# Kernel optimization log

Measured on AMD Instinct MI355X. Metric: run time of the kernel, lower is better.

The kernel has to match this reference:

```python
import jax, jax.numpy as jnp
import numpy as np
import math

B, N, C = 4, 4096, 1024
H, K_LM = 16, 256
HEAD_DIM = C // H


def setup_inputs() -> dict:
    key = jax.random.key(0)
    k1, k2, k3, k4, k5 = jax.random.split(key, 5)
    x = jax.random.normal(k1, (B, N, C), dtype=jnp.float32)
    Wqkv = jax.random.normal(k2, (3 * C, C), dtype=jnp.float32) * 0.02
    E = jax.random.normal(k3, (H, K_LM, N), dtype=jnp.float32) * 0.02
    Wproj = jax.random.normal(k4, (C, C), dtype=jnp.float32) * 0.02
    bproj = jax.random.normal(k5, (C,), dtype=jnp.float32) * 0.02
    return {"x": x, "Wqkv": Wqkv, "E": E, "Wproj": Wproj, "bproj": bproj}


def reference(x, Wqkv, E, Wproj, bproj):
    Bsz, n, c = x.shape
    h, d = H, c // H
    # qkv projection (no bias): [B,N,3C] -> (3,B,H,N,d)
    qkv = (x @ Wqkv.T).reshape(Bsz, n, 3, h, d).transpose(2, 0, 3, 1, 4)
    q, k, v = qkv[0], qkv[1], qkv[2]
    # Linformer landmark projection: E[h,k,n] @ K/V[b,h,n,d] -> [b,h,k,d]
    k_lm = jnp.einsum('hkn,bhnd->bhkd', E, k)
    v_lm = jnp.einsum('hkn,bhnd->bhkd', E, v)
    # scaled dot + softmax over landmarks: [b,h,n,k]
    dot = jnp.einsum('bhnd,bhkd->bhnk', q, k_lm) / math.sqrt(d)
    attn = jax.nn.softmax(dot, axis=-1)
    # weighted sum; faithful to original: reshape (B,H,N,d) -> (B,N,C) WITHOUT head transpose
    out = jnp.einsum('bhnk,bhkd->bhnd', attn, v_lm).reshape(Bsz, n, c)
    # output projection (dropouts are identity at eval / p=0)
    return out @ Wproj.T + bproj
```

## Files before the change

kernel.cpp:

```cpp
#include <hip/hip_runtime.h>


typedef unsigned short ushort_t;
typedef float f32x4 __attribute__((ext_vector_type(4)));
typedef __bf16 bf16x8 __attribute__((ext_vector_type(8)));
typedef unsigned short ushort8 __attribute__((ext_vector_type(8)));
typedef unsigned short ushort4_t __attribute__((ext_vector_type(4)));

__device__ inline ushort_t f2bf(float f) {
  unsigned int u = __float_as_uint(f);
  u += 0x7fff + ((u >> 16) & 1);
  return (ushort_t)(u >> 16);
}

__device__ inline void gload_lds16(const ushort_t* g, ushort_t* l) {
  __builtin_amdgcn_global_load_lds(
      (const __attribute__((address_space(1))) void*)g,
      (__attribute__((address_space(3))) void*)l, 16, 0, 0);
}

__global__ __launch_bounds__(256) void cvt_all(
    const float* __restrict__ x,  ushort_t* __restrict__ xo,
    const float* __restrict__ w1, ushort_t* __restrict__ w1o,
    const float* __restrict__ e,  ushort_t* __restrict__ eo,
    const float* __restrict__ w2, ushort_t* __restrict__ w2o) {
  int i = blockIdx.x * blockDim.x + threadIdx.x;
  const float* in; ushort_t* out; int idx;
  if (i < 4194304)               { in = x;  out = xo;  idx = i; }
  else if (i < 4980736)          { in = w1; out = w1o; idx = i - 4194304; }
  else if (i < 9175040)          { in = e;  out = eo;  idx = i - 4980736; }
  else                           { in = w2; out = w2o; idx = i - 9175040; }
  float4 v = ((const float4*)in)[idx];
  ushort4_t o;
  o.x = f2bf(v.x); o.y = f2bf(v.y); o.z = f2bf(v.z); o.w = f2bf(v.w);
  ((ushort4_t*)out)[idx] = o;
}


#define BARX __builtin_amdgcn_s_barrier()
#define WVM(n) do { asm volatile("s_waitcnt vmcnt(" #n ")" ::: "memory"); \
                    __builtin_amdgcn_sched_barrier(0); } while (0)
#define WLG  do { asm volatile("s_waitcnt lgkmcnt(0)" ::: "memory"); \
                  __builtin_amdgcn_sched_barrier(0); } while (0)

#define STG_A(h, slot, tt) do { \
    gload_lds16(sA[h][0] + (tt) * 64, (ushort_t*)(smem + (slot) * 32768 + (h) * 16384 + (w * 2 + 0) * 1024)); \
    gload_lds16(sA[h][1] + (tt) * 64, (ushort_t*)(smem + (slot) * 32768 + (h) * 16384 + (w * 2 + 1) * 1024)); \
  } while (0)
#define STG_B(h, slot, tt) do { \
    gload_lds16(sB[h][0] + (tt) * 64, (ushort_t*)(smem + 65536 + (slot) * 32768 + (h) * 16384 + (w * 2 + 0) * 1024)); \
    gload_lds16(sB[h][1] + (tt) * 64, (ushort_t*)(smem + 65536 + (slot) * 32768 + (h) * 16384 + (w * 2 + 1) * 1024)); \
  } while (0)

#define RD_A(mh, AF) do { \
    const char* ba_ = smem + sl * 32768 + ((mh) * 128 + wm * 64 + l15) * 128; \
    _Pragma("unroll") for (int i_ = 0; i_ < 4; i_++) { \
      AF[i_][0] = *(const bf16x8*)(ba_ + i_ * 2048 + cs0); \
      AF[i_][1] = *(const bf16x8*)(ba_ + i_ * 2048 + cs1); } \
  } while (0)
#define RD_B(nh) do { \
    const char* bb_ = smem + 65536 + sl * 32768 + ((nh) * 128 + wn * 32 + l15) * 128; \
    _Pragma("unroll") for (int j_ = 0; j_ < 2; j_++) { \
      bF[j_][0] = *(const bf16x8*)(bb_ + j_ * 2048 + cs0); \
      bF[j_][1] = *(const bf16x8*)(bb_ + j_ * 2048 + cs1); } \
  } while (0)

#define MQ(mh, nh, AF) do { \
    _Pragma("unroll") for (int i_ = 0; i_ < 4; i_++) \
    _Pragma("unroll") for (int j_ = 0; j_ < 2; j_++) { \
      acc[(mh) * 4 + i_][(nh) * 2 + j_] = __builtin_amdgcn_mfma_f32_16x16x32_bf16( \
          AF[i_][0], bF[j_][0], acc[(mh) * 4 + i_][(nh) * 2 + j_], 0, 0, 0); \
      acc[(mh) * 4 + i_][(nh) * 2 + j_] = __builtin_amdgcn_mfma_f32_16x16x32_bf16( \
          AF[i_][1], bF[j_][1], acc[(mh) * 4 + i_][(nh) * 2 + j_], 0, 0, 0); } \
  } while (0)

__device__ __attribute__((always_inline)) inline void pipe256(
    const ushort_t* __restrict__ Ag, const ushort_t* __restrict__ Bg,
    long long m0, long long n0, char* smem, f32x4 acc[8][4]) {
  const int tid = threadIdx.x, lane = tid & 63, w = tid >> 6;
  const int l15 = lane & 15, quad = lane >> 4;
  const int wm = w >> 2, wn = w & 3;
  const int sw = l15 & 7;
  const int K = 1024;
  const int cs0 = ((0 * 4 + quad) ^ sw) << 4;
  const int cs1 = ((1 * 4 + quad) ^ sw) << 4;
  const int lr8 = lane >> 3;
  const int sdat = ((lane & 7) ^ lr8) * 8;
  const ushort_t* sA[2][2];
  const ushort_t* sB[2][2];
#pragma unroll
  for (int h = 0; h < 2; h++)
#pragma unroll
    for (int q = 0; q < 2; q++) {
      sA[h][q] = Ag + (m0 + h * 128 + (w * 2 + q) * 8 + lr8) * K + sdat;
      sB[h][q] = Bg + (n0 + h * 128 + (w * 2 + q) * 8 + lr8) * K + sdat;
    }

  const f32x4 zz = {0.f, 0.f, 0.f, 0.f};
#pragma unroll
  for (int i = 0; i < 8; i++)
#pragma unroll
    for (int j = 0; j < 4; j++) acc[i][j] = zz;

  bf16x8 aF0[4][2];
  bf16x8 aF1[4][2];
  bf16x8 bF[2][2];

  STG_A(0, 0, 0); STG_B(0, 0, 0); STG_A(1, 0, 0); STG_B(1, 0, 0);
  WVM(4);
  BARX;

#pragma unroll 2
  for (int t = 0; t < 16; ++t) {
    const int sl = t & 1, sn = sl ^ 1;
    const bool pf = (t < 15);
    RD_A(0, aF0); RD_B(0);
    if (pf) STG_A(0, sn, t + 1);
    BARX; WLG;
    __builtin_amdgcn_s_setprio(1); MQ(0, 0, aF0); __builtin_amdgcn_s_setprio(0);
    if (pf) { WVM(4); } else { WVM(2); }
    BARX;
    RD_A(1, aF1);
    if (pf) STG_B(0, sn, t + 1);
    BARX; WLG;
    __builtin_amdgcn_s_setprio(1); MQ(1, 0, aF1); __builtin_amdgcn_s_setprio(0);
    if (pf) { WVM(4); } else { WVM(0); }
    BARX;
    RD_B(1);
    if (pf) STG_A(1, sn, t + 1);
    BARX; WLG;
    __builtin_amdgcn_s_setprio(1); MQ(1, 1, aF1); __builtin_amdgcn_s_setprio(0);
    BARX;
    if (pf) STG_B(1, sn, t + 1);
    BARX; WLG;
    __builtin_amdgcn_s_setprio(1); MQ(0, 1, aF0); __builtin_amdgcn_s_setprio(0);
    if (pf) WVM(4);
    BARX;
  }
}

__global__ __launch_bounds__(512) void gemm_qkv(
    const ushort_t* __restrict__ A, const ushort_t* __restrict__ W,
    ushort_t* __restrict__ q, ushort_t* __restrict__ kT, ushort_t* __restrict__ vT) {
  __shared__ __align__(16) char smem[131072];
  const int lin = blockIdx.x;
  const int xcd = lin & 7, rr_ = lin >> 3;
  const int mt = xcd * 8 + (rr_ & 7);
  const int nt = rr_ >> 3;
  const long long m0 = (long long)mt * 256;
  const long long n0 = (long long)nt * 256;

  f32x4 acc[8][4];
  pipe256(A, W, m0, n0, smem, acc);

  const int tid = threadIdx.x, lane = tid & 63, w = tid >> 6;
  const int l15 = lane & 15, quad = lane >> 4;
  const int wm = w >> 2, wn = w & 3;
  const int b     = (int)(m0 >> 12);
  const int nrow0 = (int)(m0 & 4095);
  const int s     = (int)(n0 >> 10);
  const int ncol0 = (int)(n0 & 1023);
  const int h0    = ncol0 >> 6;

  if (s == 0) {
#pragma unroll
    for (int mh = 0; mh < 2; mh++)
#pragma unroll
      for (int i = 0; i < 4; i++)
#pragma unroll
        for (int nh = 0; nh < 2; nh++)
#pragma unroll
          for (int j = 0; j < 2; j++) {
            int cx = ncol0 + nh * 128 + wn * 32 + j * 16;
            int h  = cx >> 6;
            int dd = (cx & 63) + l15;
            long long z = (long long)b * 16 + h;
            int nb = nrow0 + mh * 128 + wm * 64 + i * 16 + quad * 4;
#pragma unroll
            for (int r = 0; r < 4; r++)
              q[z * 262144 + (long long)(nb + r) * 64 + dd] = f2bf(acc[mh * 4 + i][nh * 2 + j][r]);
          }
  } else {
    ushort_t (*T)[136] = (ushort_t(*)[136])smem;
    ushort_t* KV = (s == 1) ? kT : vT;
#pragma unroll
    for (int p = 0; p < 2; p++) {
      __syncthreads();
#pragma unroll
      for (int i = 0; i < 4; i++)
#pragma unroll
        for (int nh = 0; nh < 2; nh++)
#pragma unroll
          for (int j = 0; j < 2; j++) {
            int c = nh * 128 + wn * 32 + j * 16 + l15;
            int t = wm * 64 + i * 16 + quad * 4;
            ushort4_t o = {f2bf(acc[p * 4 + i][nh * 2 + j][0]), f2bf(acc[p * 4 + i][nh * 2 + j][1]),
                           f2bf(acc[p * 4 + i][nh * 2 + j][2]), f2bf(acc[p * 4 + i][nh * 2 + j][3])};
            *(ushort4_t*)(&T[c][t]) = o;
          }
      __syncthreads();
#pragma unroll
      for (int it = 0; it < 8; it++) {
        int ch = it * 512 + tid;
        int cl = ch >> 4, tc = (ch & 15) * 8;
        ushort8 v = *(const ushort8*)(&T[cl][tc]);
        int h = h0 + (cl >> 6), dd = cl & 63;
        long long z = (long long)b * 16 + h;
        *(ushort8*)(KV + z * 262144 + (long long)dd * 4096 + (nrow0 + p * 128 + tc)) = v;
      }
    }
  }
}

__global__ __launch_bounds__(256) void lm_gemm(
    const ushort_t* __restrict__ E, const ushort_t* __restrict__ kT,
    const ushort_t* __restrict__ vT, float* __restrict__ pK, float* __restrict__ pV) {
  __shared__ __align__(16) ushort_t smem[12288];
  const int tid = threadIdx.x, lane = tid & 63, w = tid >> 6;
  const int l15 = lane & 15, quad = lane >> 4;
  const int lin = blockIdx.x;
  const int xcd = lin & 7, idx = lin >> 3;
  const int h   = xcd + 8 * (idx >> 6);
  const int rem = idx & 63;
  const int kt  = rem & 3;
  const int zi  = (rem >> 2) & 3;
  const int s   = rem >> 4;
  const int z   = zi * 16 + h;
  const int lr = lane >> 2;
  const int lc = ((lane & 3) ^ ((lr >> 1) & 3)) * 8;
  const int swz = (l15 >> 1) & 3;

  const ushort_t* gE = E  + ((long long)h * 256 + kt * 64 + 16 * w + lr) * 4096 + s * 1024 + lc;
  const ushort_t* gK = kT + ((long long)z * 64 + 16 * w + lr) * 4096 + s * 1024 + lc;
  const ushort_t* gV = vT + ((long long)z * 64 + 16 * w + lr) * 4096 + s * 1024 + lc;
  ushort_t* lE = smem + 512 * w;
  ushort_t* lK = smem + 4096 + 512 * w;
  ushort_t* lV = smem + 8192 + 512 * w;

  const f32x4 zz = {0.f, 0.f, 0.f, 0.f};
  f32x4 aK[4], aV[4];
#pragma unroll
  for (int j = 0; j < 4; j++) { aK[j] = zz; aV[j] = zz; }

  for (int n = 0; n < 1024; n += 64) {
    __syncthreads();
#pragma unroll
    for (int p = 0; p < 2; p++) {
      gload_lds16(gE + n + 32 * p, lE + p * 2048);
      gload_lds16(gK + n + 32 * p, lK + p * 2048);
      gload_lds16(gV + n + 32 * p, lV + p * 2048);
    }
    __syncthreads();
#pragma unroll
    for (int p = 0; p < 2; p++) {
      bf16x8 ef = *(const bf16x8*)(smem + p * 2048 + (w * 16 + l15) * 32 + ((quad ^ swz) * 8));
#pragma unroll
      for (int j = 0; j < 4; j++) {
        bf16x8 kf = *(const bf16x8*)(smem + 4096 + p * 2048 + (j * 16 + l15) * 32 + ((quad ^ swz) * 8));
        aK[j] = __builtin_amdgcn_mfma_f32_16x16x32_bf16(ef, kf, aK[j], 0, 0, 0);
        bf16x8 vf = *(const bf16x8*)(smem + 8192 + p * 2048 + (j * 16 + l15) * 32 + ((quad ^ swz) * 8));
        aV[j] = __builtin_amdgcn_mfma_f32_16x16x32_bf16(ef, vf, aV[j], 0, 0, 0);
      }
    }
  }

  float* oK = pK + ((long long)(z * 4 + s) * 256 + kt * 64) * 64;
  float* oV = pV + ((long long)(z * 4 + s) * 256 + kt * 64) * 64;
#pragma unroll
  for (int j = 0; j < 4; j++)
#pragma unroll
    for (int r = 0; r < 4; r++) {
      int row = w * 16 + quad * 4 + r, col = j * 16 + l15;
      oK[row * 64 + col] = aK[j][r];
      oV[row * 64 + col] = aV[j][r];
    }
}

__global__ __launch_bounds__(256) void lm_reduce(
    const float* __restrict__ pK, const float* __restrict__ pV,
    ushort_t* __restrict__ klm, ushort_t* __restrict__ vlmT) {
  __shared__ float Tv[64][68];
  const int tid = threadIdx.x;
  const int kt = blockIdx.x;
  const int z  = blockIdx.y;
  const long long base = (long long)z * 4 * 16384 + kt * 64 * 64;
  const int row = tid >> 2, c0 = (tid & 3) * 16;

  float sk[16];
#pragma unroll
  for (int g = 0; g < 4; g++) {
    f32x4 a = {0.f, 0.f, 0.f, 0.f};
#pragma unroll
    for (int s = 0; s < 4; s++)
      a += *(const f32x4*)(pK + base + (long long)s * 16384 + row * 64 + c0 + g * 4);
    sk[g * 4 + 0] = a[0]; sk[g * 4 + 1] = a[1]; sk[g * 4 + 2] = a[2]; sk[g * 4 + 3] = a[3];
  }
  {
    ushort_t* dst = klm + ((long long)z * 256 + kt * 64 + row) * 64 + c0;
    ushort8 o0, o1;
#pragma unroll
    for (int i = 0; i < 8; i++) { o0[i] = f2bf(sk[i]); o1[i] = f2bf(sk[8 + i]); }
    *(ushort8*)(dst) = o0;
    *(ushort8*)(dst + 8) = o1;
  }

#pragma unroll
  for (int g = 0; g < 4; g++) {
    f32x4 a = {0.f, 0.f, 0.f, 0.f};
#pragma unroll
    for (int s = 0; s < 4; s++)
      a += *(const f32x4*)(pV + base + (long long)s * 16384 + row * 64 + c0 + g * 4);
    *(f32x4*)(&Tv[row][c0 + g * 4]) = a;
  }
  __syncthreads();
  {
    ushort8 o0, o1;
#pragma unroll
    for (int i = 0; i < 8; i++) {
      o0[i] = f2bf(Tv[c0 + i][row]);
      o1[i] = f2bf(Tv[c0 + 8 + i][row]);
    }
    ushort_t* dst = vlmT + ((long long)z * 64 + row) * 256 + kt * 64 + c0;
    *(ushort8*)(dst) = o0;
    *(ushort8*)(dst + 8) = o1;
  }
}

__global__ __launch_bounds__(256) void attn_fused(
    const ushort_t* __restrict__ Q, const ushort_t* __restrict__ Klm,
    const ushort_t* __restrict__ VlmT, ushort_t* __restrict__ O) {
  __shared__ __align__(16) ushort_t smem[16896];
  ushort_t (*As)[40]  = (ushort_t(*)[40])smem;
  ushort_t (*Bs)[40]  = (ushort_t(*)[40])(smem + 2560);
  ushort_t (*P)[264]  = (ushort_t(*)[264])smem;
  const int tid = threadIdx.x, lane = tid & 63, w = tid >> 6;
  const int l15 = lane & 15, quad = lane >> 4;
  const int z = blockIdx.z;
  const long long m0 = (long long)blockIdx.x * 64;
  const ushort_t* Qb = Q + (long long)z * 262144;
  const ushort_t* Kb = Klm + (long long)z * 16384;
  const ushort_t* Vb = VlmT + (long long)z * 16384;

  const f32x4 zz = {0.f, 0.f, 0.f, 0.f};
  f32x4 acc[16];
#pragma unroll
  for (int j = 0; j < 16; j++) acc[j] = zz;

  const int sr = tid >> 2, sc = (tid & 3) * 8;

  for (int kt = 0; kt < 2; kt++) {
    const int k0 = kt * 32;
    ushort8 av = *(const ushort8*)(Qb + (m0 + sr) * 64 + k0 + sc);
    ushort8 bv[4];
#pragma unroll
    for (int r = 0; r < 4; r++) {
      int c = r * 256 + tid;
      bv[r] = *(const ushort8*)(Kb + (c >> 2) * 64 + k0 + (c & 3) * 8);
    }
    __syncthreads();
    *(ushort8*)(&As[sr][sc]) = av;
#pragma unroll
    for (int r = 0; r < 4; r++) {
      int c = r * 256 + tid;
      *(ushort8*)(&Bs[c >> 2][(c & 3) * 8]) = bv[r];
    }
    __syncthreads();
    bf16x8 af = *(const bf16x8*)(&As[w * 16 + l15][quad * 8]);
#pragma unroll
    for (int j = 0; j < 16; j++) {
      bf16x8 bfj = *(const bf16x8*)(&Bs[j * 16 + l15][quad * 8]);
      acc[j] = __builtin_amdgcn_mfma_f32_16x16x32_bf16(af, bfj, acc[j], 0, 0, 0);
    }
  }

  __syncthreads();
#pragma unroll
  for (int r = 0; r < 4; r++) {
    float x[16];
    float vmax = -1e30f;
#pragma unroll
    for (int j = 0; j < 16; j++) { x[j] = acc[j][r] * 0.125f; vmax = fmaxf(vmax, x[j]); }
#pragma unroll
    for (int m = 1; m < 16; m <<= 1) vmax = fmaxf(vmax, __shfl_xor(vmax, m, 64));
    float s = 0.f;
#pragma unroll
    for (int j = 0; j < 16; j++) { x[j] = __expf(x[j] - vmax); s += x[j]; }
#pragma unroll
    for (int m = 1; m < 16; m <<= 1) s += __shfl_xor(s, m, 64);
    float inv = 1.0f / s;
    int row = w * 16 + quad * 4 + r;
#pragma unroll
    for (int j = 0; j < 16; j++)
      P[row][j * 16 + l15] = f2bf(x[j] * inv);
  }
  __syncthreads();

  f32x4 o_acc[4];
#pragma unroll
  for (int j = 0; j < 4; j++) o_acc[j] = zz;
#pragma unroll
  for (int kc = 0; kc < 8; kc++) {
    bf16x8 pf = *(const bf16x8*)(&P[w * 16 + l15][kc * 32 + quad * 8]);
#pragma unroll
    for (int j = 0; j < 4; j++) {
      bf16x8 vf = *(const bf16x8*)(Vb + (j * 16 + l15) * 256 + kc * 32 + quad * 8);
      o_acc[j] = __builtin_amdgcn_mfma_f32_16x16x32_bf16(pf, vf, o_acc[j], 0, 0, 0);
    }
  }

#pragma unroll
  for (int j = 0; j < 4; j++)
#pragma unroll
    for (int r = 0; r < 4; r++) {
      int row = w * 16 + quad * 4 + r;
      int col = j * 16 + l15;
      O[(long long)z * 262144 + (m0 + row) * 64 + col] = f2bf(o_acc[j][r]);
    }
}

__global__ __launch_bounds__(512) void gemm_nt_256(
    const ushort_t* __restrict__ A, const ushort_t* __restrict__ B,
    float* __restrict__ C, const float* __restrict__ bias) {
  __shared__ __align__(16) char smem[131072];
  const int lin = blockIdx.x;
  const int xcd = lin & 7, rr_ = lin >> 3;
  const int mt = xcd * 8 + (rr_ & 7);
  const int nt = rr_ >> 3;
  const long long m0 = (long long)mt * 256;
  const long long n0 = (long long)nt * 256;

  f32x4 acc[8][4];
  pipe256(A, B, m0, n0, smem, acc);

  const int tid = threadIdx.x, lane = tid & 63, w = tid >> 6;
  const int l15 = lane & 15, quad = lane >> 4;
  const int wm = w >> 2, wn = w & 3;

#pragma unroll
  for (int mh = 0; mh < 2; mh++)
#pragma unroll
    for (int i = 0; i < 4; i++)
#pragma unroll
      for (int nh = 0; nh < 2; nh++)
#pragma unroll
        for (int j = 0; j < 2; j++) {
          long long row = m0 + mh * 128 + wm * 64 + i * 16 + quad * 4;
          long long col = n0 + nh * 128 + wn * 32 + j * 16 + l15;
          float bv = bias[col];
#pragma unroll
          for (int r = 0; r < 4; r++)
            C[(row + r) * 1024 + col] = acc[mh * 4 + i][nh * 2 + j][r] + bv;
        }
}

extern "C" void kernel_launch(void* const* d_in, const int* in_sizes, int n_in,
                              void* d_out, int out_size, void* d_ws, size_t ws_size,
                              hipStream_t stream) {
  const float* x     = (const float*)d_in[0];
  const float* Wqkv  = (const float*)d_in[1];
  const float* E     = (const float*)d_in[2];
  const float* Wproj = (const float*)d_in[3];
  const float* bproj = (const float*)d_in[4];
  float* out = (float*)d_out;

  char* ws = (char*)d_ws;
  ushort_t* x_bf     = (ushort_t*)(ws + 0);
  float*    pK       = (float*)   (ws + 0);
  float*    pV       = (float*)   (ws + 16777216);
  ushort_t* wqkv_bf  = (ushort_t*)(ws + 33554432);
  ushort_t* e_bf     = (ushort_t*)(ws + 39845888);
  ushort_t* wproj_bf = (ushort_t*)(ws + 73400320);
  ushort_t* q_bf     = (ushort_t*)(ws + 75497472);
  ushort_t* kT       = (ushort_t*)(ws + 109051904);
  ushort_t* vT       = (ushort_t*)(ws + 142606336);
  ushort_t* klm      = (ushort_t*)(ws + 176160768);
  ushort_t* vlmT     = (ushort_t*)(ws + 178257920);

  cvt_all<<<36864, 256, 0, stream>>>(x, x_bf, Wqkv, wqkv_bf, E, e_bf, Wproj, wproj_bf);

  gemm_qkv<<<768, 512, 0, stream>>>(x_bf, wqkv_bf, q_bf, kT, vT);

  lm_gemm<<<1024, 256, 0, stream>>>(e_bf, kT, vT, pK, pV);

  lm_reduce<<<dim3(4, 64), 256, 0, stream>>>(pK, pV, klm, vlmT);

  attn_fused<<<dim3(64, 1, 64), 256, 0, stream>>>(q_bf, klm, vlmT, x_bf);

  gemm_nt_256<<<256, 512, 0, stream>>>(x_bf, wproj_bf, out, bproj);
}
```

Baseline: 425.5 us.

## Double-buffer LDS loads in landmark GEMM to overlap global loads with MFMA

Restructures the lm_gemm main loop into a two-stage ping-pong pipeline over 32-wide k-steps. The loads for the next step are issued via global_load_lds before the MFMAs on the current buffer, using a vmcnt wait and a barrier instead of two full syncs per iteration. The goal is to hide global memory latency behind compute. It halves the per-step tile and relies on WVM/BARX macros defined elsewhere in the file.

```diff
diff --git a/kernel.cpp b/kernel.cpp
--- a/kernel.cpp
+++ b/kernel.cpp
@@ -211,6 +211,23 @@
     }
   }
 }
+
+#define LMSTG(b_, t_) do { \
+    ushort_t* base_ = smem + (b_) * 6144; \
+    gload_lds16(gE + (t_) * 32, base_ + 512 * w); \
+    gload_lds16(gK + (t_) * 32, base_ + 2048 + 512 * w); \
+    gload_lds16(gV + (t_) * 32, base_ + 4096 + 512 * w); \
+  } while (0)
+
+#define LMCMP(b_) do { \
+    const ushort_t* base_ = smem + (b_) * 6144; \
+    bf16x8 ef = *(const bf16x8*)(base_ + (w * 16 + l15) * 32 + ((quad ^ swz) * 8)); \
+    _Pragma("unroll") for (int j_ = 0; j_ < 4; j_++) { \
+      bf16x8 kf = *(const bf16x8*)(base_ + 2048 + (j_ * 16 + l15) * 32 + ((quad ^ swz) * 8)); \
+      aK[j_] = __builtin_amdgcn_mfma_f32_16x16x32_bf16(ef, kf, aK[j_], 0, 0, 0); \
+      bf16x8 vf = *(const bf16x8*)(base_ + 4096 + (j_ * 16 + l15) * 32 + ((quad ^ swz) * 8)); \
+      aV[j_] = __builtin_amdgcn_mfma_f32_16x16x32_bf16(ef, vf, aV[j_], 0, 0, 0); \
+    } } while (0)
 
 __global__ __launch_bounds__(256) void lm_gemm(
     const ushort_t* __restrict__ E, const ushort_t* __restrict__ kT,
@@ -233,36 +250,25 @@
   const ushort_t* gE = E  + ((long long)h * 256 + kt * 64 + 16 * w + lr) * 4096 + s * 1024 + lc;
   const ushort_t* gK = kT + ((long long)z * 64 + 16 * w + lr) * 4096 + s * 1024 + lc;
   const ushort_t* gV = vT + ((long long)z * 64 + 16 * w + lr) * 4096 + s * 1024 + lc;
-  ushort_t* lE = smem + 512 * w;
-  ushort_t* lK = smem + 4096 + 512 * w;
-  ushort_t* lV = smem + 8192 + 512 * w;
 
   const f32x4 zz = {0.f, 0.f, 0.f, 0.f};
   f32x4 aK[4], aV[4];
 #pragma unroll
   for (int j = 0; j < 4; j++) { aK[j] = zz; aV[j] = zz; }
 
-  for (int n = 0; n < 1024; n += 64) {
-    __syncthreads();
-#pragma unroll
-    for (int p = 0; p < 2; p++) {
-      gload_lds16(gE + n + 32 * p, lE + p * 2048);
-      gload_lds16(gK + n + 32 * p, lK + p * 2048);
-      gload_lds16(gV + n + 32 * p, lV + p * 2048);
-    }
-    __syncthreads();
-#pragma unroll
-    for (int p = 0; p < 2; p++) {
-      bf16x8 ef = *(const bf16x8*)(smem + p * 2048 + (w * 16 + l15) * 32 + ((quad ^ swz) * 8));
-#pragma unroll
-      for (int j = 0; j < 4; j++) {
-        bf16x8 kf = *(const bf16x8*)(smem + 4096 + p * 2048 + (j * 16 + l15) * 32 + ((quad ^ swz) * 8));
-        aK[j] = __builtin_amdgcn_mfma_f32_16x16x32_bf16(ef, kf, aK[j], 0, 0, 0);
-        bf16x8 vf = *(const bf16x8*)(smem + 8192 + p * 2048 + (j * 16 + l15) * 32 + ((quad ^ swz) * 8));
-        aV[j] = __builtin_amdgcn_mfma_f32_16x16x32_bf16(ef, vf, aV[j], 0, 0, 0);
-      }
-    }
-  }
+  LMSTG(0, 0);
+#pragma unroll 2
+  for (int t = 0; t < 31; ++t) {
+    const int b = t & 1;
+    LMSTG(b ^ 1, t + 1);
+    WVM(3);
+    BARX;
+    LMCMP(b);
+    BARX;
+  }
+  WVM(0);
+  BARX;
+  LMCMP(1);
 
   float* oK = pK + ((long long)(z * 4 + s) * 256 + kt * 64) * 64;
   float* oV = pV + ((long long)(z * 4 + s) * 256 + kt * 64) * 64;
```

Result: no change. 420.9 us (-1.1%).
